# Optimization experiments

Measured on AMD Instinct MI355X. Metric: run time of the kernel, lower is better.

Reference implementation:

```python
import jax, jax.numpy as jnp
from jax import lax
import numpy as np

B, M = 16384, 200            # flattened batch (B*TT), tokens per observation
NUM_LAYERS, GW, GH = 22, 11, 11
CNN_CH, HIDDEN = 128, 512
ACTION_NVEC = (9, 10)

MAX_VEC = jnp.array([9.0, 1.0, 1.0, 10.0, 3.0, 254.0, 1.0, 1.0, 235.0, 8.0, 9.0,
                     250.0, 29.0, 1.0, 1.0, 8.0, 1.0, 1.0, 6.0, 3.0, 1.0, 2.0],
                    jnp.float32)[None, :, None, None]  # [1,22,1,1]


def setup_inputs() -> dict:
    key = jax.random.key(0)
    ks = jax.random.split(key, 16)
    # compose coords byte so x,y nibbles are valid grid indices (0..10)
    xs = jax.random.randint(ks[0], (B, M), 0, GW)
    ys = jax.random.randint(ks[1], (B, M), 0, GH)
    coords = xs * 16 + ys
    atr = jax.random.randint(ks[2], (B, M), 0, NUM_LAYERS)
    val = jax.random.randint(ks[3], (B, M), 0, 11)
    observations = jnp.stack([coords, atr, val], axis=-1).astype(jnp.int32)  # [B,M,3]

    def nrm(k, shape, std=0.02):
        return (jax.random.normal(k, shape, jnp.float32) * std)

    return {
        "observations": observations,
        "conv1_w": nrm(ks[4], (CNN_CH, NUM_LAYERS, 5, 5)),
        "conv1_b": jnp.zeros((CNN_CH,), jnp.float32),
        "conv2_w": nrm(ks[5], (CNN_CH, CNN_CH, 3, 3)),
        "conv2_b": jnp.zeros((CNN_CH,), jnp.float32),
        "fc_w": nrm(ks[6], (HIDDEN // 2, CNN_CH)),
        "fc_b": jnp.zeros((HIDDEN // 2,), jnp.float32),
        "self_w": nrm(ks[7], (HIDDEN // 2, NUM_LAYERS)),
        "self_b": jnp.zeros((HIDDEN // 2,), jnp.float32),
        "actor0_w": nrm(ks[8], (ACTION_NVEC[0], HIDDEN), std=0.01),
        "actor0_b": jnp.zeros((ACTION_NVEC[0],), jnp.float32),
        "actor1_w": nrm(ks[9], (ACTION_NVEC[1], HIDDEN), std=0.01),
        "actor1_b": jnp.zeros((ACTION_NVEC[1],), jnp.float32),
        "value_w": nrm(ks[10], (1, HIDDEN)),
        "value_b": jnp.zeros((1,), jnp.float32),
    }


def reference(observations, conv1_w, conv1_b, conv2_w, conv2_b, fc_w, fc_b,
              self_w, self_b, actor0_w, actor0_b, actor1_w, actor1_b,
              value_w, value_b):
    obs = jnp.where(observations == 255, 0, observations)
    coords = obs[..., 0]
    xs = (coords >> 4) & 15
    ys = coords & 15
    atr = obs[..., 1]
    vals = obs[..., 2].astype(jnp.float32)           # [B,M]
    Bt = obs.shape[0]
    b_idx = jnp.broadcast_to(jnp.arange(Bt)[:, None], vals.shape)
    # masked scatter into dense grid (all tokens valid after 255->0 clamp)
    box = jnp.zeros((Bt, NUM_LAYERS, GW, GH), jnp.float32)
    box = box.at[b_idx, atr, xs, ys].set(vals, mode="drop")
    feats = box / MAX_VEC                            # [B,22,11,11]

    self_f = jax.nn.relu(feats[:, :, 5, 5] @ self_w.T + self_b)  # [B,256]

    dn = ("NCHW", "OIHW", "NCHW")
    h = lax.conv_general_dilated(feats, conv1_w, (3, 3), "VALID", dimension_numbers=dn)
    h = jax.nn.relu(h + conv1_b[None, :, None, None])            # [B,128,3,3]
    h = lax.conv_general_dilated(h, conv2_w, (1, 1), "VALID", dimension_numbers=dn)
    h = jax.nn.relu(h + conv2_b[None, :, None, None])            # [B,128,1,1]
    h = h.reshape(Bt, -1)
    cnn_f = jax.nn.relu(h @ fc_w.T + fc_b)                       # [B,256]

    hidden = jnp.concatenate([self_f, cnn_f], axis=1)            # [B,512]
    logits0 = hidden @ actor0_w.T + actor0_b
    logits1 = hidden @ actor1_w.T + actor1_b
    value = hidden @ value_w.T + value_b
    return (logits0, logits1, value)
```

## Files before the change

kernel.cpp:

```cpp
#include <hip/hip_runtime.h>

typedef unsigned short u16;
typedef __attribute__((ext_vector_type(8))) short short8;
typedef __attribute__((ext_vector_type(4))) float f32x4;

#define MFMA16(a, b, c) __builtin_amdgcn_mfma_f32_16x16x32_bf16((a), (b), (c), 0, 0, 0)

__device__ __forceinline__ u16 f2bf(float f) {
    unsigned u = __float_as_uint(f);
    unsigned r = (u + 0x7FFFu + ((u >> 16) & 1u)) >> 16;
    return (u16)r;
}

__device__ const float MAXV[22] = {9.f, 1.f, 1.f, 10.f, 3.f, 254.f, 1.f, 1.f, 235.f, 8.f, 9.f,
                                   250.f, 29.f, 1.f, 1.f, 8.f, 1.f, 1.f, 6.f, 3.f, 1.f, 2.f};

__global__ void prep_kernel(
    const float* c1w, const float* c1b, const float* c2w, const float* c2b,
    const float* fcw, const float* fcb, const float* sfw, const float* sfb,
    const float* a0w, const float* a0b, const float* a1w, const float* a1b,
    const float* vw, const float* vb,
    u16* W1F, u16* W2F, u16* FCF, u16* SELFF, u16* HEADF, float* BIAS)
{
    int idx = blockIdx.x * 256 + threadIdx.x;
    if (idx < 73728) {
        int grp = idx >> 9, off = idx & 511;
        int g = grp / 18, ks = grp - g * 18;
        int l = off >> 3, e = off & 7;
        int n = g * 16 + (l & 15);
        int k = ks * 32 + ((l >> 4) << 3) + e;
        float v = 0.f;
        if (k < 550) { int c = k / 25; v = c1w[n * 550 + k] * (1.0f / MAXV[c]); }
        W1F[idx] = f2bf(v);
    } else if (idx < 221184) {
        int j = idx - 73728;
        int grp = j >> 9, off = j & 511;
        int g = grp / 36, ks = grp - g * 36;
        int l = off >> 3, e = off & 7;
        int oc = g * 16 + (l & 15);
        int k = ks * 32 + ((l >> 4) << 3) + e;
        W2F[j] = f2bf(c2w[oc * 1152 + (k & 127) * 9 + (k >> 7)]);
    } else if (idx < 253952) {
        int j = idx - 221184;
        int grp = j >> 9, off = j & 511;
        int g = grp >> 2, kc = grp & 3;
        int l = off >> 3, e = off & 7;
        int n = g * 16 + (l & 15);
        int k = kc * 32 + ((l >> 4) << 3) + e;
        FCF[j] = f2bf(fcw[n * 128 + k]);
    } else if (idx < 262144) {
        int j = idx - 253952;
        int g = j >> 9, off = j & 511;
        int l = off >> 3, e = off & 7;
        int n = g * 16 + (l & 15);
        int k = ((l >> 4) << 3) + e;
        float v = (k < 22) ? sfw[n * 22 + k] * (1.0f / MAXV[k]) : 0.f;
        SELFF[j] = f2bf(v);
    } else if (idx < 278528) {
        int j = idx - 262144;
        int grp = j >> 9, off = j & 511;
        int g = grp >> 4, ks = grp & 15;
        int l = off >> 3, e = off & 7;
        int n = g * 16 + (l & 15);
        int k = ks * 32 + ((l >> 4) << 3) + e;
        float v = 0.f;
        if (n < 9) v = a0w[n * 512 + k];
        else if (n < 19) v = a1w[(n - 9) * 512 + k];
        else if (n == 19) v = vw[k];
        HEADF[j] = f2bf(v);
    } else if (idx < 279328) {
        int j = idx - 278528;
        float v = 0.f;
        if (j < 128) v = c1b[j];
        else if (j < 256) v = c2b[j - 128];
        else if (j < 512) v = fcb[j - 256];
        else if (j < 768) v = sfb[j - 512];
        else {
            int j2 = j - 768;
            if (j2 < 9) v = a0b[j2]; else if (j2 < 19) v = a1b[j2 - 9]; else if (j2 == 19) v = vb[0];
        }
        BIAS[j] = v;
    }
}

__global__ __launch_bounds__(256, 3) void k12_kernel(
    const int* __restrict__ obs, const u16* __restrict__ W1F,
    const float* __restrict__ BIAS, u16* __restrict__ h1F, u16* __restrict__ s22g)
{
    __shared__ __align__(16) u16 A[36 * 576];
    __shared__ __align__(16) int box[2664];
    __shared__ u16 s22[128];
    const int tid = threadIdx.x, w = tid >> 6, l = tid & 63;
    const int s0 = blockIdx.x * 4;

    int tok[4][3];
    if (tid < 200) {
        #pragma unroll
        for (int p = 0; p < 4; ++p) {
            const int* tp = obs + (long)(s0 + p) * 600 + tid * 3;
            tok[p][0] = tp[0]; tok[p][1] = tp[1]; tok[p][2] = tp[2];
        }
    }

    {
        short8 z = {0, 0, 0, 0, 0, 0, 0, 0};
        for (int i = tid; i < 2592; i += 256) *(short8*)(A + i * 8) = z;
        int4 zz = {0, 0, 0, 0};
        for (int i = tid; i < 666; i += 256) ((int4*)box)[i] = zz;
        if (tid < 128) s22[tid] = 0;
    }
    __syncthreads();

    #pragma unroll
    for (int p = 0; p < 4; ++p) {
        int ce = 0, en = 0, va = 0, xa = 0, ya = 0, aa = 0, ok = 0;
        if (tid < 200) {
            int c = tok[p][0], a = tok[p][1], v = tok[p][2];
            c = (c == 255) ? 0 : c; a = (a == 255) ? 0 : a; v = (v == 255) ? 0 : v;
            int xs = (c >> 4) & 15, ys = c & 15;
            ok = ((unsigned)a < 22u) & (xs < 11) & (ys < 11);
            ce = a * 121 + xs * 11 + ys;
            en = ((p + 1) << 16) | (tid << 8) | (v & 255);
            va = v; xa = xs; ya = ys; aa = a;
            if (ok) atomicMax(&box[ce], en);
        }
        __syncthreads();
        if (ok && box[ce] == en) {
            u16 bv = f2bf((float)va);
            if (xa == 5 && ya == 5) s22[p * 32 + aa] = bv;
            int bcol = aa * 25;
            #pragma unroll
            for (int ox = 0; ox < 3; ++ox) {
                int kx = xa - 3 * ox;
                if ((unsigned)kx > 4u) continue;
                #pragma unroll
                for (int oy = 0; oy < 3; ++oy) {
                    int ky = ya - 3 * oy;
                    if ((unsigned)ky > 4u) continue;
                    int row = p * 9 + ox * 3 + oy;
                    int byte = ((row * 576 + bcol + kx * 5 + ky) << 1) ^ ((row & 7) << 4);
                    *(u16*)((char*)A + byte) = bv;
                }
            }
        }
        __syncthreads();
    }
    if (tid < 128) s22g[s0 * 32 + tid] = s22[tid];

    int Aoff[3][2];
    #pragma unroll
    for (int mt = 0; mt < 3; ++mt) {
        int row = mt * 16 + (l & 15);
        row = row < 36 ? row : 35;
        int koff = (l >> 4) << 3;
        Aoff[mt][0] = ((row * 576 + koff) << 1) ^ ((row & 7) << 4);
        Aoff[mt][1] = ((row * 576 + 32 + koff) << 1) ^ ((row & 7) << 4);
    }
    const u16* Wp0 = W1F + ((w * 2 + 0) * 18 << 9) + l * 8;
    const u16* Wp1 = W1F + ((w * 2 + 1) * 18 << 9) + l * 8;

    f32x4 acc[3][2];
    const f32x4 fz = {0.f, 0.f, 0.f, 0.f};
    #pragma unroll
    for (int i = 0; i < 3; ++i) { acc[i][0] = fz; acc[i][1] = fz; }

    short8 cb0 = *(const short8*)(Wp0);
    short8 cb1 = *(const short8*)(Wp1);
    short8 nb0 = *(const short8*)(Wp0 + 512);
    short8 nb1 = *(const short8*)(Wp1 + 512);
    __builtin_amdgcn_s_setprio(1);
    #pragma unroll
    for (int ks = 0; ks < 18; ++ks) {
        short8 t0 = cb0, t1 = cb1;
        if (ks < 16) {
            t0 = *(const short8*)(Wp0 + (ks + 2) * 512);
            t1 = *(const short8*)(Wp1 + (ks + 2) * 512);
        }
        short8 a0 = *(const short8*)((const char*)A + Aoff[0][ks & 1] + (ks >> 1) * 128);
        short8 a1 = *(const short8*)((const char*)A + Aoff[1][ks & 1] + (ks >> 1) * 128);
        short8 a2 = *(const short8*)((const char*)A + Aoff[2][ks & 1] + (ks >> 1) * 128);
        acc[0][0] = MFMA16(a0, cb0, acc[0][0]);
        acc[0][1] = MFMA16(a0, cb1, acc[0][1]);
        acc[1][0] = MFMA16(a1, cb0, acc[1][0]);
        acc[1][1] = MFMA16(a1, cb1, acc[1][1]);
        acc[2][0] = MFMA16(a2, cb0, acc[2][0]);
        acc[2][1] = MFMA16(a2, cb1, acc[2][1]);
        cb0 = nb0; cb1 = nb1; nb0 = t0; nb1 = t1;
    }
    __builtin_amdgcn_s_setprio(0);

    u16* R = (u16*)box;
    #pragma unroll
    for (int mt = 0; mt < 3; ++mt) {
        #pragma unroll
        for (int nt = 0; nt < 2; ++nt) {
            int col = w * 32 + nt * 16 + (l & 15);
            float bias = BIAS[col];
            int hif = nt * 2 + ((l & 15) >> 3);
            int ef = l & 7;
            #pragma unroll
            for (int r = 0; r < 4; ++r) {
                int row = mt * 16 + ((l >> 4) << 2) + r;
                if (row < 36) {
                    int ds = row / 9;
                    int pos = row - ds * 9;
                    int ks = pos * 4 + w;
                    float v = acc[mt][nt][r] + bias;
                    v = v > 0.f ? v : 0.f;
                    R[(ks * 16 + hif * 4 + ds) * 8 + ef] = f2bf(v);
                }
            }
        }
    }
    __syncthreads();
    {
        const long Cbase = (long)(s0 >> 4) * 18432 + (s0 & 15) * 8;
        #pragma unroll
        for (int q = 0; q < 3; ++q) {
            int slot = tid + q * 256;
            if (slot < 576) {
                int ks = slot >> 4, lf = slot & 15;
                *(short8*)(h1F + Cbase + ks * 512 + (lf >> 2) * 128 + (lf & 3) * 8) =
                    *(const short8*)(R + slot * 8);
            }
        }
    }
}

__global__ __launch_bounds__(256, 2) void k3_kernel(
    const u16* __restrict__ h1F, const u16* __restrict__ s22g,
    const u16* __restrict__ W2F, const u16* __restrict__ FCF,
    const u16* __restrict__ SELFF, const u16* __restrict__ HEADF,
    const float* __restrict__ BIAS, float* __restrict__ out, int B)
{
    __shared__ __align__(16) u16 A3[32 * 136];
    __shared__ __align__(16) u16 HID[32 * 520];
    const int tid = threadIdx.x, w = tid >> 6, l = tid & 63;
    const int s0 = blockIdx.x * 32;
    const int sb = blockIdx.x * 2;
    const float* c2b = BIAS + 128;
    const float* fcb = BIAS + 256;
    const float* sfb = BIAS + 512;
    const float* hdb = BIAS + 768;
    const f32x4 fz = {0.f, 0.f, 0.f, 0.f};

    f32x4 acc[2][2];
    acc[0][0] = fz; acc[0][1] = fz; acc[1][0] = fz; acc[1][1] = fz;
    const u16* A0p = h1F + (long)(sb + 0) * 18432 + l * 8;
    const u16* A1p = h1F + (long)(sb + 1) * 18432 + l * 8;
    const u16* B0p = W2F + ((w * 2 + 0) * 36 << 9) + l * 8;
    const u16* B1p = W2F + ((w * 2 + 1) * 36 << 9) + l * 8;

    short8 ca0 = *(const short8*)(A0p), ca1 = *(const short8*)(A1p);
    short8 cb0 = *(const short8*)(B0p), cb1 = *(const short8*)(B1p);
    short8 na0 = *(const short8*)(A0p + 512), na1 = *(const short8*)(A1p + 512);
    short8 nb0 = *(const short8*)(B0p + 512), nb1 = *(const short8*)(B1p + 512);
    __builtin_amdgcn_s_setprio(1);
    #pragma unroll
    for (int ks = 0; ks < 36; ++ks) {
        short8 t0 = ca0, t1 = ca1, t2 = cb0, t3 = cb1;
        if (ks < 34) {
            t0 = *(const short8*)(A0p + (ks + 2) * 512);
            t1 = *(const short8*)(A1p + (ks + 2) * 512);
            t2 = *(const short8*)(B0p + (ks + 2) * 512);
            t3 = *(const short8*)(B1p + (ks + 2) * 512);
        }
        acc[0][0] = MFMA16(ca0, cb0, acc[0][0]);
        acc[0][1] = MFMA16(ca0, cb1, acc[0][1]);
        acc[1][0] = MFMA16(ca1, cb0, acc[1][0]);
        acc[1][1] = MFMA16(ca1, cb1, acc[1][1]);
        ca0 = na0; ca1 = na1; cb0 = nb0; cb1 = nb1;
        na0 = t0; na1 = t1; nb0 = t2; nb1 = t3;
    }
    __builtin_amdgcn_s_setprio(0);
    {
        #pragma unroll
        for (int mt = 0; mt < 2; ++mt)
            #pragma unroll
            for (int nt = 0; nt < 2; ++nt) {
                int col = w * 32 + nt * 16 + (l & 15);
                float bias = c2b[col];
                #pragma unroll
                for (int r = 0; r < 4; ++r) {
                    int row = mt * 16 + ((l >> 4) << 2) + r;
                    float v = acc[mt][nt][r] + bias; v = v > 0.f ? v : 0.f;
                    A3[row * 136 + col] = f2bf(v);
                }
            }
    }
    __syncthreads();

    f32x4 acc8[2][4];
    #pragma unroll
    for (int i = 0; i < 2; ++i)
        #pragma unroll
        for (int j = 0; j < 4; ++j) acc8[i][j] = fz;
    #pragma unroll
    for (int kc = 0; kc < 4; ++kc) {
        short8 bf[4];
        #pragma unroll
        for (int nt = 0; nt < 4; ++nt)
            bf[nt] = *(const short8*)(FCF + (((w * 4 + nt) * 4 + kc) << 9) + l * 8);
        #pragma unroll
        for (int mt = 0; mt < 2; ++mt) {
            short8 a = *(const short8*)(A3 + (mt * 16 + (l & 15)) * 136 + kc * 32 + ((l >> 4) << 3));
            #pragma unroll
            for (int nt = 0; nt < 4; ++nt) acc8[mt][nt] = MFMA16(a, bf[nt], acc8[mt][nt]);
        }
    }
    {
        #pragma unroll
        for (int mt = 0; mt < 2; ++mt)
            #pragma unroll
            for (int nt = 0; nt < 4; ++nt) {
                int col = w * 64 + nt * 16 + (l & 15);
                float bias = fcb[col];
                #pragma unroll
                for (int r = 0; r < 4; ++r) {
                    int row = mt * 16 + ((l >> 4) << 2) + r;
                    float v = acc8[mt][nt][r] + bias; v = v > 0.f ? v : 0.f;
                    HID[row * 520 + 256 + col] = f2bf(v);
                }
            }
    }

    {
        f32x4 acc9[2][4];
        #pragma unroll
        for (int i = 0; i < 2; ++i)
            #pragma unroll
            for (int j = 0; j < 4; ++j) acc9[i][j] = fz;
        short8 bs[4];
        #pragma unroll
        for (int nt = 0; nt < 4; ++nt)
            bs[nt] = *(const short8*)(SELFF + ((w * 4 + nt) << 9) + l * 8);
        #pragma unroll
        for (int mt = 0; mt < 2; ++mt) {
            short8 a = *(const short8*)(s22g + (s0 + mt * 16 + (l & 15)) * 32 + ((l >> 4) << 3));
            #pragma unroll
            for (int nt = 0; nt < 4; ++nt) acc9[mt][nt] = MFMA16(a, bs[nt], acc9[mt][nt]);
        }
        #pragma unroll
        for (int mt = 0; mt < 2; ++mt)
            #pragma unroll
            for (int nt = 0; nt < 4; ++nt) {
                int col = w * 64 + nt * 16 + (l & 15);
                float bias = sfb[col];
                #pragma unroll
                for (int r = 0; r < 4; ++r) {
                    int row = mt * 16 + ((l >> 4) << 2) + r;
                    float v = acc9[mt][nt][r] + bias; v = v > 0.f ? v : 0.f;
                    HID[row * 520 + col] = f2bf(v);
                }
            }
    }
    __syncthreads();

    f32x4 hacc = fz;
    const int rt = w & 1, ct = w >> 1;
    #pragma unroll
    for (int ks = 0; ks < 16; ++ks) {
        short8 a = *(const short8*)(HID + (rt * 16 + (l & 15)) * 520 + ks * 32 + ((l >> 4) << 3));
        short8 b = *(const short8*)(HEADF + ((ct * 16 + ks) << 9) + l * 8);
        hacc = MFMA16(a, b, hacc);
    }
    #pragma unroll
    for (int r = 0; r < 4; ++r) {
        int srow = s0 + rt * 16 + ((l >> 4) << 2) + r;
        int col = ct * 16 + (l & 15);
        float v = hacc[r] + hdb[col];
        if (col < 9) out[(long)srow * 9 + col] = v;
        else if (col < 19) out[(long)B * 9 + (long)srow * 10 + (col - 9)] = v;
        else if (col == 19) out[(long)B * 19 + srow] = v;
    }
}

extern "C" void kernel_launch(void* const* d_in, const int* in_sizes, int n_in,
                              void* d_out, int out_size, void* d_ws, size_t ws_size,
                              hipStream_t stream)
{
    const int*   obs = (const int*)d_in[0];
    const float* c1w = (const float*)d_in[1];
    const float* c1b = (const float*)d_in[2];
    const float* c2w = (const float*)d_in[3];
    const float* c2b = (const float*)d_in[4];
    const float* fcw = (const float*)d_in[5];
    const float* fcb = (const float*)d_in[6];
    const float* sfw = (const float*)d_in[7];
    const float* sfb = (const float*)d_in[8];
    const float* a0w = (const float*)d_in[9];
    const float* a0b = (const float*)d_in[10];
    const float* a1w = (const float*)d_in[11];
    const float* a1b = (const float*)d_in[12];
    const float* vw  = (const float*)d_in[13];
    const float* vb  = (const float*)d_in[14];
    const int B = in_sizes[0] / 600;

    char* ws = (char*)d_ws;
    u16*   W1F   = (u16*)(ws + 0);
    u16*   W2F   = (u16*)(ws + 147456);
    u16*   FCF   = (u16*)(ws + 442368);
    u16*   SELFF = (u16*)(ws + 507904);
    u16*   HEADF = (u16*)(ws + 524288);
    float* BIAS  = (float*)(ws + 557056);
    u16*   s22g  = (u16*)(ws + 560256);
    u16*   h1F   = (u16*)(ws + 560256 + (size_t)B * 64);

    prep_kernel<<<1092, 256, 0, stream>>>(c1w, c1b, c2w, c2b, fcw, fcb, sfw, sfb,
                                          a0w, a0b, a1w, a1b, vw, vb,
                                          W1F, W2F, FCF, SELFF, HEADF, BIAS);
    k12_kernel<<<B / 4, 256, 0, stream>>>(obs, W1F, BIAS, h1F, s22g);
    k3_kernel<<<B / 32, 256, 0, stream>>>(h1F, s22g, W2F, FCF, SELFF, HEADF, BIAS,
                                          (float*)d_out, B);
}
```

Measured before the change: 75.94 us.

## Split conv2 into separate kernel and halve samples per conv1 block

The conv1 kernel now handles two samples per block instead of four, which shrinks LDS use and raises the launch-bounds occupancy target. The h1 intermediate layout changes to a simpler per-block contiguous format. Conv2 is moved into its own kernel that processes 64 samples per block, so each W2 fragment is reused across more rows. It writes a new a3 intermediate buffer that a second kernel consumes for the fc, self and head layers. The split adds an extra launch and a global round trip for the conv2 activations.

New measurement: 97.58 us. +28.5%, slower.

```diff
diff --git a/kernel.cpp b/kernel.cpp
--- a/kernel.cpp
+++ b/kernel.cpp
@@ -83,36 +83,35 @@
     }
 }
 
-__global__ __launch_bounds__(256, 3) void k12_kernel(
+__global__ __launch_bounds__(256, 5) void k12_kernel(
     const int* __restrict__ obs, const u16* __restrict__ W1F,
     const float* __restrict__ BIAS, u16* __restrict__ h1F, u16* __restrict__ s22g)
 {
-    __shared__ __align__(16) u16 A[36 * 576];
+    __shared__ __align__(16) u16 A[18 * 576];
     __shared__ __align__(16) int box[2664];
-    __shared__ u16 s22[128];
+    __shared__ u16 s22[64];
     const int tid = threadIdx.x, w = tid >> 6, l = tid & 63;
-    const int s0 = blockIdx.x * 4;
-
-    int tok[4][3];
+    const int s0 = blockIdx.x * 2;
+
+    int tok[2][3];
     if (tid < 200) {
         #pragma unroll
-        for (int p = 0; p < 4; ++p) {
+        for (int p = 0; p < 2; ++p) {
             const int* tp = obs + (long)(s0 + p) * 600 + tid * 3;
             tok[p][0] = tp[0]; tok[p][1] = tp[1]; tok[p][2] = tp[2];
         }
     }
-
     {
         short8 z = {0, 0, 0, 0, 0, 0, 0, 0};
-        for (int i = tid; i < 2592; i += 256) *(short8*)(A + i * 8) = z;
+        for (int i = tid; i < 1296; i += 256) *(short8*)(A + i * 8) = z;
         int4 zz = {0, 0, 0, 0};
         for (int i = tid; i < 666; i += 256) ((int4*)box)[i] = zz;
-        if (tid < 128) s22[tid] = 0;
+        if (tid < 64) s22[tid] = 0;
     }
     __syncthreads();
 
     #pragma unroll
-    for (int p = 0; p < 4; ++p) {
+    for (int p = 0; p < 2; ++p) {
         int ce = 0, en = 0, va = 0, xa = 0, ya = 0, aa = 0, ok = 0;
         if (tid < 200) {
             int c = tok[p][0], a = tok[p][1], v = tok[p][2];
@@ -145,13 +144,13 @@
         }
         __syncthreads();
     }
-    if (tid < 128) s22g[s0 * 32 + tid] = s22[tid];
-
-    int Aoff[3][2];
-    #pragma unroll
-    for (int mt = 0; mt < 3; ++mt) {
+    if (tid < 64) s22g[s0 * 32 + tid] = s22[tid];
+
+    int Aoff[2][2];
+    #pragma unroll
+    for (int mt = 0; mt < 2; ++mt) {
         int row = mt * 16 + (l & 15);
-        row = row < 36 ? row : 35;
+        row = row < 18 ? row : 17;
         int koff = (l >> 4) << 3;
         Aoff[mt][0] = ((row * 576 + koff) << 1) ^ ((row & 7) << 4);
         Aoff[mt][1] = ((row * 576 + 32 + koff) << 1) ^ ((row & 7) << 4);
@@ -159,10 +158,9 @@
     const u16* Wp0 = W1F + ((w * 2 + 0) * 18 << 9) + l * 8;
     const u16* Wp1 = W1F + ((w * 2 + 1) * 18 << 9) + l * 8;
 
-    f32x4 acc[3][2];
+    f32x4 acc[2][2];
     const f32x4 fz = {0.f, 0.f, 0.f, 0.f};
-    #pragma unroll
-    for (int i = 0; i < 3; ++i) { acc[i][0] = fz; acc[i][1] = fz; }
+    acc[0][0] = fz; acc[0][1] = fz; acc[1][0] = fz; acc[1][1] = fz;
 
     short8 cb0 = *(const short8*)(Wp0);
     short8 cb1 = *(const short8*)(Wp1);
@@ -178,151 +176,158 @@
         }
         short8 a0 = *(const short8*)((const char*)A + Aoff[0][ks & 1] + (ks >> 1) * 128);
         short8 a1 = *(const short8*)((const char*)A + Aoff[1][ks & 1] + (ks >> 1) * 128);
-        short8 a2 = *(const short8*)((const char*)A + Aoff[2][ks & 1] + (ks >> 1) * 128);
         acc[0][0] = MFMA16(a0, cb0, acc[0][0]);
         acc[0][1] = MFMA16(a0, cb1, acc[0][1]);
         acc[1][0] = MFMA16(a1, cb0, acc[1][0]);
         acc[1][1] = MFMA16(a1, cb1, acc[1][1]);
-        acc[2][0] = MFMA16(a2, cb0, acc[2][0]);
-        acc[2][1] = MFMA16(a2, cb1, acc[2][1]);
         cb0 = nb0; cb1 = nb1; nb0 = t0; nb1 = t1;
     }
     __builtin_amdgcn_s_setprio(0);
 
     u16* R = (u16*)box;
     #pragma unroll
-    for (int mt = 0; mt < 3; ++mt) {
+    for (int mt = 0; mt < 2; ++mt) {
         #pragma unroll
         for (int nt = 0; nt < 2; ++nt) {
             int col = w * 32 + nt * 16 + (l & 15);
             float bias = BIAS[col];
-            int hif = nt * 2 + ((l & 15) >> 3);
-            int ef = l & 7;
+            int kosub = (nt * 2 + ((l & 15) >> 3)) * 8 + (l & 7);
             #pragma unroll
             for (int r = 0; r < 4; ++r) {
                 int row = mt * 16 + ((l >> 4) << 2) + r;
-                if (row < 36) {
-                    int ds = row / 9;
-                    int pos = row - ds * 9;
-                    int ks = pos * 4 + w;
+                if (row < 18) {
+                    int ls = row / 9, pos = row - ls * 9;
                     float v = acc[mt][nt][r] + bias;
                     v = v > 0.f ? v : 0.f;
-                    R[(ks * 16 + hif * 4 + ds) * 8 + ef] = f2bf(v);
+                    R[(pos * 4 + w) * 64 + ls * 32 + kosub] = f2bf(v);
                 }
             }
         }
     }
     __syncthreads();
     {
-        const long Cbase = (long)(s0 >> 4) * 18432 + (s0 & 15) * 8;
-        #pragma unroll
-        for (int q = 0; q < 3; ++q) {
+        #pragma unroll
+        for (int q = 0; q < 2; ++q) {
             int slot = tid + q * 256;
-            if (slot < 576) {
-                int ks = slot >> 4, lf = slot & 15;
-                *(short8*)(h1F + Cbase + ks * 512 + (lf >> 2) * 128 + (lf & 3) * 8) =
-                    *(const short8*)(R + slot * 8);
+            if (slot < 288)
+                *(short8*)(h1F + (long)blockIdx.x * 2304 + slot * 8) = *(const short8*)(R + slot * 8);
+        }
+    }
+}
+
+__global__ __launch_bounds__(256, 4) void k3a_kernel(
+    const u16* __restrict__ h1F, const u16* __restrict__ W2F,
+    const float* __restrict__ BIAS, u16* __restrict__ a3F)
+{
+    const int tid = threadIdx.x, w = tid >> 6, l = tid & 63;
+    const int s0 = blockIdx.x * 64;
+    const float* c2b = BIAS + 128;
+    const f32x4 fz = {0.f, 0.f, 0.f, 0.f};
+    f32x4 acc[4][2];
+    #pragma unroll
+    for (int i = 0; i < 4; ++i) { acc[i][0] = fz; acc[i][1] = fz; }
+
+    const u16* Ap[4];
+    #pragma unroll
+    for (int mt = 0; mt < 4; ++mt) {
+        int s = s0 + mt * 16 + (l & 15);
+        Ap[mt] = h1F + (long)(s >> 1) * 2304 + (s & 1) * 32 + ((l >> 4) << 3);
+    }
+    const u16* B0p = W2F + ((w * 2 + 0) * 36 << 9) + l * 8;
+    const u16* B1p = W2F + ((w * 2 + 1) * 36 << 9) + l * 8;
+
+    short8 ca[4], na[4], cb0, cb1, nb0, nb1;
+    #pragma unroll
+    for (int mt = 0; mt < 4; ++mt) { ca[mt] = *(const short8*)(Ap[mt]); na[mt] = *(const short8*)(Ap[mt] + 64); }
+    cb0 = *(const short8*)(B0p); cb1 = *(const short8*)(B1p);
+    nb0 = *(const short8*)(B0p + 512); nb1 = *(const short8*)(B1p + 512);
+    __builtin_amdgcn_s_setprio(1);
+    #pragma unroll
+    for (int ks = 0; ks < 36; ++ks) {
+        short8 ta[4], tb0 = cb0, tb1 = cb1;
+        #pragma unroll
+        for (int mt = 0; mt < 4; ++mt) ta[mt] = ca[mt];
+        if (ks < 34) {
+            #pragma unroll
+            for (int mt = 0; mt < 4; ++mt) ta[mt] = *(const short8*)(Ap[mt] + (ks + 2) * 64);
+            tb0 = *(const short8*)(B0p + (ks + 2) * 512);
+            tb1 = *(const short8*)(B1p + (ks + 2) * 512);
+        }
+        #pragma unroll
+        for (int mt = 0; mt < 4; ++mt) {
+            acc[mt][0] = MFMA16(ca[mt], cb0, acc[mt][0]);
+            acc[mt][1] = MFMA16(ca[mt], cb1, acc[mt][1]);
+        }
+        #pragma unroll
+        for (int mt = 0; mt < 4; ++mt) { ca[mt] = na[mt]; na[mt] = ta[mt]; }
+        cb0 = nb0; cb1 = nb1; nb0 = tb0; nb1 = tb1;
+    }
+    __builtin_amdgcn_s_setprio(0);
+
+    #pragma unroll
+    for (int mt = 0; mt < 4; ++mt) {
+        #pragma unroll
+        for (int nt = 0; nt < 2; ++nt) {
+            int col = w * 32 + nt * 16 + (l & 15);
+            float bias = c2b[col];
+            #pragma unroll
+            for (int r = 0; r < 4; ++r) {
+                int row = mt * 16 + ((l >> 4) << 2) + r;
+                int s = s0 + row;
+                float v = acc[mt][nt][r] + bias; v = v > 0.f ? v : 0.f;
+                long ad = (long)(s >> 4) * 2048 + (col >> 5) * 512 +
+                          (s & 15) * 8 + (((col >> 3) & 3) << 7) + (col & 7);
+                a3F[ad] = f2bf(v);
             }
         }
     }
 }
 
-__global__ __launch_bounds__(256, 2) void k3_kernel(
-    const u16* __restrict__ h1F, const u16* __restrict__ s22g,
-    const u16* __restrict__ W2F, const u16* __restrict__ FCF,
-    const u16* __restrict__ SELFF, const u16* __restrict__ HEADF,
-    const float* __restrict__ BIAS, float* __restrict__ out, int B)
+__global__ __launch_bounds__(256, 4) void k3b_kernel(
+    const u16* __restrict__ a3F, const u16* __restrict__ s22g,
+    const u16* __restrict__ FCF, const u16* __restrict__ SELFF,
+    const u16* __restrict__ HEADF, const float* __restrict__ BIAS,
+    float* __restrict__ out, int B)
 {
-    __shared__ __align__(16) u16 A3[32 * 136];
     __shared__ __align__(16) u16 HID[32 * 520];
     const int tid = threadIdx.x, w = tid >> 6, l = tid & 63;
     const int s0 = blockIdx.x * 32;
-    const int sb = blockIdx.x * 2;
-    const float* c2b = BIAS + 128;
     const float* fcb = BIAS + 256;
     const float* sfb = BIAS + 512;
     const float* hdb = BIAS + 768;
     const f32x4 fz = {0.f, 0.f, 0.f, 0.f};
 
-    f32x4 acc[2][2];
-    acc[0][0] = fz; acc[0][1] = fz; acc[1][0] = fz; acc[1][1] = fz;
-    const u16* A0p = h1F + (long)(sb + 0) * 18432 + l * 8;
-    const u16* A1p = h1F + (long)(sb + 1) * 18432 + l * 8;
-    const u16* B0p = W2F + ((w * 2 + 0) * 36 << 9) + l * 8;
-    const u16* B1p = W2F + ((w * 2 + 1) * 36 << 9) + l * 8;
-
-    short8 ca0 = *(const short8*)(A0p), ca1 = *(const short8*)(A1p);
-    short8 cb0 = *(const short8*)(B0p), cb1 = *(const short8*)(B1p);
-    short8 na0 = *(const short8*)(A0p + 512), na1 = *(const short8*)(A1p + 512);
-    short8 nb0 = *(const short8*)(B0p + 512), nb1 = *(const short8*)(B1p + 512);
-    __builtin_amdgcn_s_setprio(1);
-    #pragma unroll
-    for (int ks = 0; ks < 36; ++ks) {
-        short8 t0 = ca0, t1 = ca1, t2 = cb0, t3 = cb1;
-        if (ks < 34) {
-            t0 = *(const short8*)(A0p + (ks + 2) * 512);
-            t1 = *(const short8*)(A1p + (ks + 2) * 512);
-            t2 = *(const short8*)(B0p + (ks + 2) * 512);
-            t3 = *(const short8*)(B1p + (ks + 2) * 512);
-        }
-        acc[0][0] = MFMA16(ca0, cb0, acc[0][0]);
-        acc[0][1] = MFMA16(ca0, cb1, acc[0][1]);
-        acc[1][0] = MFMA16(ca1, cb0, acc[1][0]);
-        acc[1][1] = MFMA16(ca1, cb1, acc[1][1]);
-        ca0 = na0; ca1 = na1; cb0 = nb0; cb1 = nb1;
-        na0 = t0; na1 = t1; nb0 = t2; nb1 = t3;
-    }
-    __builtin_amdgcn_s_setprio(0);
-    {
+    f32x4 acc8[2][4];
+    #pragma unroll
+    for (int i = 0; i < 2; ++i)
+        #pragma unroll
+        for (int j = 0; j < 4; ++j) acc8[i][j] = fz;
+    #pragma unroll
+    for (int kc = 0; kc < 4; ++kc) {
+        short8 a[2];
         #pragma unroll
         for (int mt = 0; mt < 2; ++mt)
-            #pragma unroll
-            for (int nt = 0; nt < 2; ++nt) {
-                int col = w * 32 + nt * 16 + (l & 15);
-                float bias = c2b[col];
-                #pragma unroll
-                for (int r = 0; r < 4; ++r) {
-                    int row = mt * 16 + ((l >> 4) << 2) + r;
-                    float v = acc[mt][nt][r] + bias; v = v > 0.f ? v : 0.f;
-                    A3[row * 136 + col] = f2bf(v);
-                }
+            a[mt] = *(const short8*)(a3F + (long)blockIdx.x * 4096 + mt * 2048 + kc * 512 + l * 8);
+        #pragma unroll
+        for (int nt = 0; nt < 4; ++nt) {
+            short8 bf = *(const short8*)(FCF + (((w * 4 + nt) * 4 + kc) << 9) + l * 8);
+            acc8[0][nt] = MFMA16(a[0], bf, acc8[0][nt]);
+            acc8[1][nt] = MFMA16(a[1], bf, acc8[1][nt]);
+        }
+    }
+    #pragma unroll
+    for (int mt = 0; mt < 2; ++mt)
+        #pragma unroll
+        for (int nt = 0; nt < 4; ++nt) {
+            int col = w * 64 + nt * 16 + (l & 15);
+            float bias = fcb[col];
+            #pragma unroll
+            for (int r = 0; r < 4; ++r) {
+                int row = mt * 16 + ((l >> 4) << 2) + r;
+                float v = acc8[mt][nt][r] + bias; v = v > 0.f ? v : 0.f;
+                HID[row * 520 + 256 + col] = f2bf(v);
             }
-    }
-    __syncthreads();
-
-    f32x4 acc8[2][4];
-    #pragma unroll
-    for (int i = 0; i < 2; ++i)
-        #pragma unroll
-        for (int j = 0; j < 4; ++j) acc8[i][j] = fz;
-    #pragma unroll
-    for (int kc = 0; kc < 4; ++kc) {
-        short8 bf[4];
-        #pragma unroll
-        for (int nt = 0; nt < 4; ++nt)
-            bf[nt] = *(const short8*)(FCF + (((w * 4 + nt) * 4 + kc) << 9) + l * 8);
-        #pragma unroll
-        for (int mt = 0; mt < 2; ++mt) {
-            short8 a = *(const short8*)(A3 + (mt * 16 + (l & 15)) * 136 + kc * 32 + ((l >> 4) << 3));
-            #pragma unroll
-            for (int nt = 0; nt < 4; ++nt) acc8[mt][nt] = MFMA16(a, bf[nt], acc8[mt][nt]);
-        }
-    }
-    {
-        #pragma unroll
-        for (int mt = 0; mt < 2; ++mt)
-            #pragma unroll
-            for (int nt = 0; nt < 4; ++nt) {
-                int col = w * 64 + nt * 16 + (l & 15);
-                float bias = fcb[col];
-                #pragma unroll
-                for (int r = 0; r < 4; ++r) {
-                    int row = mt * 16 + ((l >> 4) << 2) + r;
-                    float v = acc8[mt][nt][r] + bias; v = v > 0.f ? v : 0.f;
-                    HID[row * 520 + 256 + col] = f2bf(v);
-                }
-            }
-    }
+        }
 
     {
         f32x4 acc9[2][4];
@@ -330,15 +335,15 @@
         for (int i = 0; i < 2; ++i)
             #pragma unroll
             for (int j = 0; j < 4; ++j) acc9[i][j] = fz;
-        short8 bs[4];
-        #pragma unroll
-        for (int nt = 0; nt < 4; ++nt)
-            bs[nt] = *(const short8*)(SELFF + ((w * 4 + nt) << 9) + l * 8);
-        #pragma unroll
-        for (int mt = 0; mt < 2; ++mt) {
-            short8 a = *(const short8*)(s22g + (s0 + mt * 16 + (l & 15)) * 32 + ((l >> 4) << 3));
-            #pragma unroll
-            for (int nt = 0; nt < 4; ++nt) acc9[mt][nt] = MFMA16(a, bs[nt], acc9[mt][nt]);
+        short8 a[2];
+        #pragma unroll
+        for (int mt = 0; mt < 2; ++mt)
+            a[mt] = *(const short8*)(s22g + (s0 + mt * 16 + (l & 15)) * 32 + ((l >> 4) << 3));
+        #pragma unroll
+        for (int nt = 0; nt < 4; ++nt) {
+            short8 bs = *(const short8*)(SELFF + ((w * 4 + nt) << 9) + l * 8);
+            acc9[0][nt] = MFMA16(a[0], bs, acc9[0][nt]);
+            acc9[1][nt] = MFMA16(a[1], bs, acc9[1][nt]);
         }
         #pragma unroll
         for (int mt = 0; mt < 2; ++mt)
@@ -356,22 +361,24 @@
     }
     __syncthreads();
 
-    f32x4 hacc = fz;
-    const int rt = w & 1, ct = w >> 1;
-    #pragma unroll
-    for (int ks = 0; ks < 16; ++ks) {
-        short8 a = *(const short8*)(HID + (rt * 16 + (l & 15)) * 520 + ks * 32 + ((l >> 4) << 3));
-        short8 b = *(const short8*)(HEADF + ((ct * 16 + ks) << 9) + l * 8);
-        hacc = MFMA16(a, b, hacc);
-    }
-    #pragma unroll
-    for (int r = 0; r < 4; ++r) {
-        int srow = s0 + rt * 16 + ((l >> 4) << 2) + r;
-        int col = ct * 16 + (l & 15);
-        float v = hacc[r] + hdb[col];
-        if (col < 9) out[(long)srow * 9 + col] = v;
-        else if (col < 19) out[(long)B * 9 + (long)srow * 10 + (col - 9)] = v;
-        else if (col == 19) out[(long)B * 19 + srow] = v;
+    {
+        f32x4 hacc = fz;
+        const int mt = w & 1, ct = w >> 1;
+        #pragma unroll
+        for (int ks = 0; ks < 16; ++ks) {
+            short8 a = *(const short8*)(HID + (mt * 16 + (l & 15)) * 520 + ks * 32 + ((l >> 4) << 3));
+            short8 b = *(const short8*)(HEADF + ((ct * 16 + ks) << 9) + l * 8);
+            hacc = MFMA16(a, b, hacc);
+        }
+        #pragma unroll
+        for (int r = 0; r < 4; ++r) {
+            int srow = s0 + mt * 16 + ((l >> 4) << 2) + r;
+            int col = ct * 16 + (l & 15);
+            float v = hacc[r] + hdb[col];
+            if (col < 9) out[(long)srow * 9 + col] = v;
+            else if (col < 19) out[(long)B * 9 + (long)srow * 10 + (col - 9)] = v;
+            else if (col == 19) out[(long)B * 19 + srow] = v;
+        }
     }
 }
 
@@ -405,11 +412,13 @@
     float* BIAS  = (float*)(ws + 557056);
     u16*   s22g  = (u16*)(ws + 560256);
     u16*   h1F   = (u16*)(ws + 560256 + (size_t)B * 64);
+    u16*   a3F   = (u16*)(ws + 560256 + (size_t)B * 64 + (size_t)B * 2304);
 
     prep_kernel<<<1092, 256, 0, stream>>>(c1w, c1b, c2w, c2b, fcw, fcb, sfw, sfb,
                                           a0w, a0b, a1w, a1b, vw, vb,
                                           W1F, W2F, FCF, SELFF, HEADF, BIAS);
-    k12_kernel<<<B / 4, 256, 0, stream>>>(obs, W1F, BIAS, h1F, s22g);
-    k3_kernel<<<B / 32, 256, 0, stream>>>(h1F, s22g, W2F, FCF, SELFF, HEADF, BIAS,
-                                          (float*)d_out, B);
-}
+    k12_kernel<<<B / 2, 256, 0, stream>>>(obs, W1F, BIAS, h1F, s22g);
+    k3a_kernel<<<B / 64, 256, 0, stream>>>(h1F, W2F, BIAS, a3F);
+    k3b_kernel<<<B / 32, 256, 0, stream>>>(a3F, s22g, FCF, SELFF, HEADF, BIAS,
+                                           (float*)d_out, B);
+}
```
